# Performance work log

Measured on AMD Instinct MI355X. Metric: run time of the kernel, lower is better.

## Reference

```python
import jax, jax.numpy as jnp
import numpy as np

N_P, N_A, N_T = 20000, 10000, 5000
D_IN, D_OUT = 512, 256
E_P, E_A, E_T = 320000, 160000, 80000


def setup_inputs() -> dict:
    key = jax.random.key(0)
    ks = iter(jax.random.split(key, 64))

    def nrm(shape, scale=1.0):
        return jax.random.normal(next(ks), shape, dtype=jnp.float32) * scale

    def xav(shape):
        # xavier_uniform-like scale (gain 1.414), normal draw is fine for a baseline
        return nrm(shape, 1.414 * (2.0 / (shape[0] + shape[1])) ** 0.5)

    def edges(ne, n_src, n_dst):
        src = jax.random.randint(next(ks), (ne,), 0, n_src, dtype=jnp.int32)
        dst = jax.random.randint(next(ks), (ne,), 0, n_dst, dtype=jnp.int32)
        w = jax.random.uniform(next(ks), (ne,), dtype=jnp.float32) / 16.0  # ~normalized adj values
        return src, dst, w

    d = {}
    d["x_p"] = nrm((N_P, D_IN))
    d["x_a"] = nrm((N_A, D_IN))
    d["x_t"] = nrm((N_T, D_IN))
    d["e_p_a_src"], d["e_p_a_dst"], d["e_p_a_w"] = edges(E_P, N_A, N_P)
    d["e_p_t_src"], d["e_p_t_dst"], d["e_p_t_w"] = edges(E_P, N_T, N_P)
    d["e_a_p_src"], d["e_a_p_dst"], d["e_a_p_w"] = edges(E_A, N_P, N_A)
    d["e_a_t_src"], d["e_a_t_dst"], d["e_a_t_w"] = edges(E_A, N_T, N_A)
    d["e_t_p_src"], d["e_t_p_dst"], d["e_t_p_w"] = edges(E_T, N_P, N_T)
    d["e_t_a_src"], d["e_t_a_dst"], d["e_t_a_w"] = edges(E_T, N_A, N_T)
    # parameters for each target type k: W_proj per neighbor, w_self, w_share, w_att, w_cat, bias
    for k, nbs in (("p", ("a", "t")), ("a", ("p", "t")), ("t", ("p", "a"))):
        for nb in nbs:
            d[f"W_{k}_{nb}"] = xav((D_IN, D_OUT))
        d[f"ws_{k}"] = xav((D_IN, D_OUT))
        d[f"wsh_{k}"] = xav((D_OUT, D_OUT))
        d[f"watt_{k}"] = xav((2 * D_OUT, 1))
        d[f"wcat_{k}"] = xav((2 * D_OUT, D_OUT))
        d[f"b_{k}"] = xav((1, D_OUT))
    return d


def _hete_agg(x_self, w_self, w_share, w_att, w_cat, bias, nb_inputs):
    """nb_inputs: list of (x_nb, W_proj, src, dst, edge_w). Faithful to HeteAggregateLayer."""
    n = x_self.shape[0]
    self_ft = (x_self @ w_self) @ w_share  # [n, d]
    # per-relation: project -> spmm (gather + weighted segment-sum over dst) -> share
    nb_fts = [
        jax.ops.segment_sum((x_nb @ Wp)[src] * ew[:, None], dst, num_segments=n) @ w_share
        for (x_nb, Wp, src, dst, ew) in nb_inputs
    ]
    L = len(nb_fts)
    # e = leaky_relu(cat([cat(nb_ft,0), self_ft.repeat(L,1)],1) @ w_att)  -> [L*n, 1]
    e = jnp.concatenate(
        [jax.nn.leaky_relu(jnp.concatenate([f, self_ft], axis=1) @ w_att) for f in nb_fts],
        axis=0,
    )
    # NOTE: faithful replication of the original `e.view(-1, L)` reshape semantics
    att = jax.nn.softmax(e.reshape(n, L), axis=1)  # [n, L]
    agg = nb_fts[0] * att[:, 0:1]
    for i in range(1, L):
        agg = agg + nb_fts[i] * att[:, i : i + 1]
    return jnp.concatenate([agg, self_ft], axis=1) @ w_cat + bias


def reference(x_p, x_a, x_t,
              e_p_a_src, e_p_a_dst, e_p_a_w, e_p_t_src, e_p_t_dst, e_p_t_w,
              e_a_p_src, e_a_p_dst, e_a_p_w, e_a_t_src, e_a_t_dst, e_a_t_w,
              e_t_p_src, e_t_p_dst, e_t_p_w, e_t_a_src, e_t_a_dst, e_t_a_w,
              W_p_a, W_p_t, ws_p, wsh_p, watt_p, wcat_p, b_p,
              W_a_p, W_a_t, ws_a, wsh_a, watt_a, wcat_a, b_a,
              W_t_p, W_t_a, ws_t, wsh_t, watt_t, wcat_t, b_t):
    out_p = _hete_agg(x_p, ws_p, wsh_p, watt_p, wcat_p, b_p,
                      [(x_a, W_p_a, e_p_a_src, e_p_a_dst, e_p_a_w),
                       (x_t, W_p_t, e_p_t_src, e_p_t_dst, e_p_t_w)])
    out_a = _hete_agg(x_a, ws_a, wsh_a, watt_a, wcat_a, b_a,
                      [(x_p, W_a_p, e_a_p_src, e_a_p_dst, e_a_p_w),
                       (x_t, W_a_t, e_a_t_src, e_a_t_dst, e_a_t_w)])
    out_t = _hete_agg(x_t, ws_t, wsh_t, watt_t, wcat_t, b_t,
                      [(x_p, W_t_p, e_t_p_src, e_t_p_dst, e_t_p_w),
                       (x_a, W_t_a, e_t_a_src, e_t_a_dst, e_t_a_w)])
    return (out_p, out_a, out_t)
```

## Files before the change

### kernel.cpp

```cpp
#include <hip/hip_runtime.h>

namespace {

typedef short s16x8 __attribute__((ext_vector_type(8)));
typedef float f32x4 __attribute__((ext_vector_type(4)));

__device__ __forceinline__ float bf2f(unsigned short u) {
  return __uint_as_float(((unsigned)u) << 16);
}
__device__ __forceinline__ unsigned short f2bf(float f) {
  unsigned u = __float_as_uint(f);
  u += 0x7fffu + ((u >> 16) & 1u);
  return (unsigned short)(u >> 16);
}

struct Tc6 { const float* src[6]; unsigned short* dst[6]; int R[6]; };
__global__ __launch_bounds__(256) void transpose_cvt(Tc6 a) {
  int mat = blockIdx.z;
  int R = a.R[mat];
  int r0 = blockIdx.y * 32, c0 = blockIdx.x * 32;
  if (r0 >= R) return;
  const float* __restrict__ src = a.src[mat];
  unsigned short* __restrict__ dst = a.dst[mat];
  __shared__ float T[32][33];
  int tx = threadIdx.x & 31, ty = threadIdx.x >> 5;
  #pragma unroll
  for (int j = 0; j < 4; ++j) {
    int r = ty + j * 8;
    T[r][tx] = src[(size_t)(r0 + r) * 256 + c0 + tx];
  }
  __syncthreads();
  #pragma unroll
  for (int j = 0; j < 4; ++j) {
    int c = ty + j * 8;
    dst[(size_t)(c0 + c) * R + r0 + tx] = f2bf(T[tx][c]);
  }
}

struct Comb9 { const unsigned short* A[9]; const float* B[9]; unsigned short* C[9]; };
__global__ __launch_bounds__(256) void combine_mfma(Comb9 g) {
  int z = blockIdx.z;
  const unsigned short* __restrict__ A = g.A[z];
  const float* __restrict__ B = g.B[z];
  unsigned short* __restrict__ C = g.C[z];
  int row0 = blockIdx.y * 128;
  int col0 = blockIdx.x * 128;
  __shared__ unsigned short As[128 * 40];
  __shared__ unsigned short Bs[128 * 40];
  int tid = threadIdx.x, lane = tid & 63, w = tid >> 6;
  int quad = lane >> 4, m16 = lane & 15;
  f32x4 acc[2][8];
  #pragma unroll
  for (int r = 0; r < 2; ++r)
    #pragma unroll
    for (int c = 0; c < 8; ++c) acc[r][c] = (f32x4){0.f, 0.f, 0.f, 0.f};
  for (int k0 = 0; k0 < 256; k0 += 32) {
    #pragma unroll
    for (int i = 0; i < 2; ++i) {
      int ch = tid + i * 256;
      int m = ch >> 2, kk = (ch & 3) * 8;
      *(s16x8*)&As[m * 40 + kk] = *(const s16x8*)(A + (size_t)(row0 + m) * 256 + k0 + kk);
      const float4* bp = (const float4*)(B + (size_t)(col0 + m) * 256 + k0 + kk);
      float4 b0 = bp[0], b1 = bp[1];
      s16x8 bv;
      bv[0] = (short)f2bf(b0.x); bv[1] = (short)f2bf(b0.y);
      bv[2] = (short)f2bf(b0.z); bv[3] = (short)f2bf(b0.w);
      bv[4] = (short)f2bf(b1.x); bv[5] = (short)f2bf(b1.y);
      bv[6] = (short)f2bf(b1.z); bv[7] = (short)f2bf(b1.w);
      *(s16x8*)&Bs[m * 40 + kk] = bv;
    }
    __syncthreads();
    s16x8 af[2], bf[8];
    #pragma unroll
    for (int r = 0; r < 2; ++r)
      af[r] = *(const s16x8*)&As[(w * 32 + r * 16 + m16) * 40 + quad * 8];
    #pragma unroll
    for (int c = 0; c < 8; ++c)
      bf[c] = *(const s16x8*)&Bs[(c * 16 + m16) * 40 + quad * 8];
    #pragma unroll
    for (int r = 0; r < 2; ++r)
      #pragma unroll
      for (int c = 0; c < 8; ++c)
        acc[r][c] = __builtin_amdgcn_mfma_f32_16x16x32_bf16(af[r], bf[c], acc[r][c], 0, 0, 0);
    __syncthreads();
  }
  #pragma unroll
  for (int r = 0; r < 2; ++r)
    #pragma unroll
    for (int i = 0; i < 4; ++i) {
      int row = row0 + w * 32 + r * 16 + quad * 4 + i;
      #pragma unroll
      for (int c = 0; c < 8; ++c)
        C[(size_t)row * 512 + col0 + c * 16 + m16] = f2bf(acc[r][c][i]);
    }
}

struct Proj9 { const float* A[9]; const unsigned short* Bt[9]; unsigned short* C[9]; int M[9]; };
__global__ __launch_bounds__(256, 3) void proj_mfma9(Proj9 g) {
  int z = blockIdx.z;
  int M = g.M[z];
  int row0 = blockIdx.y * 64;
  if (row0 >= M) return;
  const float* __restrict__ A = g.A[z];
  const unsigned short* __restrict__ Bt = g.Bt[z];
  unsigned short* __restrict__ C = g.C[z];
  __shared__ unsigned short As[64 * 40];
  __shared__ unsigned short Bs[256 * 40];
  int tid = threadIdx.x, lane = tid & 63, w = tid >> 6;
  int quad = lane >> 4, m16 = lane & 15;
  int am = tid >> 2, akk = (tid & 3) * 8;
  int gr = row0 + am;
  f32x4 acc[4][4];
  #pragma unroll
  for (int r = 0; r < 4; ++r)
    #pragma unroll
    for (int c = 0; c < 4; ++c) acc[r][c] = (f32x4){0.f, 0.f, 0.f, 0.f};

  float4 pa0 = {}, pa1 = {};
  s16x8 pb[4];

  if (gr < M) {
    const float4* ap = (const float4*)(A + (size_t)gr * 512 + akk);
    pa0 = ap[0]; pa1 = ap[1];
  }
  #pragma unroll
  for (int i = 0; i < 4; ++i) {
    int ch = tid + i * 256;
    int m = ch >> 2, kk = (ch & 3) * 8;
    pb[i] = *(const s16x8*)(Bt + (size_t)m * 512 + kk);
  }
  {
    s16x8 v;
    v[0] = (short)f2bf(pa0.x); v[1] = (short)f2bf(pa0.y);
    v[2] = (short)f2bf(pa0.z); v[3] = (short)f2bf(pa0.w);
    v[4] = (short)f2bf(pa1.x); v[5] = (short)f2bf(pa1.y);
    v[6] = (short)f2bf(pa1.z); v[7] = (short)f2bf(pa1.w);
    *(s16x8*)&As[am * 40 + akk] = v;
    #pragma unroll
    for (int i = 0; i < 4; ++i) {
      int ch = tid + i * 256;
      int m = ch >> 2, kk = (ch & 3) * 8;
      *(s16x8*)&Bs[m * 40 + kk] = pb[i];
    }
  }
  __syncthreads();

  for (int k0 = 0; k0 < 512; k0 += 32) {
    int kn = k0 + 32;
    if (kn < 512) {
      if (gr < M) {
        const float4* ap = (const float4*)(A + (size_t)gr * 512 + kn + akk);
        pa0 = ap[0]; pa1 = ap[1];
      }
      #pragma unroll
      for (int i = 0; i < 4; ++i) {
        int ch = tid + i * 256;
        int m = ch >> 2, kk = (ch & 3) * 8;
        pb[i] = *(const s16x8*)(Bt + (size_t)m * 512 + kn + kk);
      }
    }
    s16x8 af[4], bf[4];
    #pragma unroll
    for (int r = 0; r < 4; ++r)
      af[r] = *(const s16x8*)&As[(r * 16 + m16) * 40 + quad * 8];
    #pragma unroll
    for (int c = 0; c < 4; ++c)
      bf[c] = *(const s16x8*)&Bs[(w * 64 + c * 16 + m16) * 40 + quad * 8];
    #pragma unroll
    for (int r = 0; r < 4; ++r)
      #pragma unroll
      for (int c = 0; c < 4; ++c)
        acc[r][c] = __builtin_amdgcn_mfma_f32_16x16x32_bf16(af[r], bf[c], acc[r][c], 0, 0, 0);
    __syncthreads();
    if (kn < 512) {
      s16x8 v;
      v[0] = (short)f2bf(pa0.x); v[1] = (short)f2bf(pa0.y);
      v[2] = (short)f2bf(pa0.z); v[3] = (short)f2bf(pa0.w);
      v[4] = (short)f2bf(pa1.x); v[5] = (short)f2bf(pa1.y);
      v[6] = (short)f2bf(pa1.z); v[7] = (short)f2bf(pa1.w);
      *(s16x8*)&As[am * 40 + akk] = v;
      #pragma unroll
      for (int i = 0; i < 4; ++i) {
        int ch = tid + i * 256;
        int m = ch >> 2, kk = (ch & 3) * 8;
        *(s16x8*)&Bs[m * 40 + kk] = pb[i];
      }
      __syncthreads();
    }
  }
  #pragma unroll
  for (int r = 0; r < 4; ++r)
    #pragma unroll
    for (int i = 0; i < 4; ++i) {
      int row = row0 + r * 16 + quad * 4 + i;
      if (row < M) {
        #pragma unroll
        for (int c = 0; c < 4; ++c)
          C[(size_t)row * 256 + w * 64 + c * 16 + m16] = f2bf(acc[r][c][i]);
      }
    }
}

struct Edges6 { const int* src[6]; const int* dst[6]; const float* w[6]; int nE[6]; int cbase[6]; };

__global__ __launch_bounds__(256) void hist_all(Edges6 ep, int* __restrict__ counts) {
  int rho = blockIdx.y;
  int e = blockIdx.x * 256 + threadIdx.x;
  if (e >= ep.nE[rho]) return;
  atomicAdd(&counts[ep.cbase[rho] + ep.dst[rho][e]], 1);
}

__global__ __launch_bounds__(256) void scan1(const int* __restrict__ cnt, int* __restrict__ out,
                                             int* __restrict__ part, int len) {
  __shared__ int sh[256];
  int base = blockIdx.x * 2048 + threadIdx.x * 8;
  int v[8];
  int s = 0;
  #pragma unroll
  for (int j = 0; j < 8; ++j) {
    int i = base + j;
    int x = (i < len) ? cnt[i] : 0;
    v[j] = s;
    s += x;
  }
  sh[threadIdx.x] = s;
  __syncthreads();
  for (int off = 1; off < 256; off <<= 1) {
    int t = (threadIdx.x >= off) ? sh[threadIdx.x - off] : 0;
    __syncthreads();
    sh[threadIdx.x] += t;
    __syncthreads();
  }
  int texcl = sh[threadIdx.x] - s;
  #pragma unroll
  for (int j = 0; j < 8; ++j) {
    int i = base + j;
    if (i < len) out[i] = texcl + v[j];
  }
  if (threadIdx.x == 255) part[blockIdx.x] = sh[255];
}

__global__ void scan2(int* __restrict__ part, int nb, int* __restrict__ total_out) {
  __shared__ int sh[64];
  int t = threadIdx.x;
  int v = (t < nb) ? part[t] : 0;
  sh[t] = v;
  __syncthreads();
  for (int off = 1; off < 64; off <<= 1) {
    int x = (t >= off) ? sh[t - off] : 0;
    __syncthreads();
    sh[t] += x;
    __syncthreads();
  }
  if (t < nb) part[t] = sh[t] - v;
  if (t == 63) *total_out = sh[63];
}

__global__ __launch_bounds__(256) void scan3(int* __restrict__ offs, int* __restrict__ cursor,
                                             const int* __restrict__ part, int len) {
  int i = blockIdx.x * 256 + threadIdx.x;
  if (i >= len) return;
  int v = offs[i] + part[i >> 11];
  offs[i] = v;
  cursor[i] = v;
}

__global__ __launch_bounds__(256) void fill_all(Edges6 ep, int* __restrict__ cursor,
                                                unsigned int* __restrict__ pay) {
  int rho = blockIdx.y;
  int e = blockIdx.x * 256 + threadIdx.x;
  if (e >= ep.nE[rho]) return;
  int pos = atomicAdd(&cursor[ep.cbase[rho] + ep.dst[rho][e]], 1);
  pay[pos] = (((unsigned)f2bf(ep.w[rho][e])) << 16) | (unsigned)ep.src[rho][e];
}

struct Gather6 { const unsigned short* proj[6]; unsigned short* out[6]; int cb[6]; int n[6]; };
__global__ __launch_bounds__(256) void gather_all(Gather6 g, const int* __restrict__ offs,
                                                  const unsigned int* __restrict__ pay) {
  int rho = blockIdx.y;
  int n = g.n[rho];
  int d = blockIdx.x * 4 + (threadIdx.x >> 6);
  if (d >= n) return;
  int lane = threadIdx.x & 63, half = lane >> 5, l32 = lane & 31;
  const unsigned short* __restrict__ proj = g.proj[rho];
  const int* of = offs + g.cb[rho];
  int s0 = of[d], s1 = of[d + 1];
  float acc[8] = {};
  int e = s0 + half;
  for (; e + 2 < s1; e += 4) {
    unsigned int u0 = pay[e], u1 = pay[e + 2];
    float wt0 = bf2f((unsigned short)(u0 >> 16));
    float wt1 = bf2f((unsigned short)(u1 >> 16));
    s16x8 v0 = *(const s16x8*)(proj + (size_t)(u0 & 0xffffu) * 256 + l32 * 8);
    s16x8 v1 = *(const s16x8*)(proj + (size_t)(u1 & 0xffffu) * 256 + l32 * 8);
    #pragma unroll
    for (int j = 0; j < 8; ++j) {
      acc[j] = fmaf(bf2f((unsigned short)v0[j]), wt0, acc[j]);
      acc[j] = fmaf(bf2f((unsigned short)v1[j]), wt1, acc[j]);
    }
  }
  if (e < s1) {
    unsigned int u = pay[e];
    float wt = bf2f((unsigned short)(u >> 16));
    s16x8 v = *(const s16x8*)(proj + (size_t)(u & 0xffffu) * 256 + l32 * 8);
    #pragma unroll
    for (int j = 0; j < 8; ++j) acc[j] = fmaf(bf2f((unsigned short)v[j]), wt, acc[j]);
  }
  #pragma unroll
  for (int j = 0; j < 8; ++j) acc[j] += __shfl(acc[j], lane ^ 32, 64);
  if (half == 0) {
    s16x8 o;
    #pragma unroll
    for (int j = 0; j < 8; ++j) o[j] = (short)f2bf(acc[j]);
    *(s16x8*)(g.out[rho] + (size_t)d * 256 + l32 * 8) = o;
  }
}

struct Att3 { const unsigned short* nb[3]; const unsigned short* self[3];
              const float* watt[3]; float* att[3]; int n[3]; };
__global__ __launch_bounds__(256) void e_att3(Att3 g) {
  int z = blockIdx.z;
  int n = g.n[z];
  int wv = threadIdx.x >> 6;
  int idx = blockIdx.x * 4 + wv;
  int lane = threadIdx.x & 63;
  __shared__ float ev[4];
  float sum = 0.f;
  if (idx < 2 * n) {
    int i = idx < n ? idx : idx - n;
    ushort4 v  = *(const ushort4*)(g.nb[z] + (size_t)idx * 256 + (lane << 2));
    ushort4 sv = *(const ushort4*)(g.self[z] + (size_t)i * 256 + (lane << 2));
    float4 wa = *(const float4*)(g.watt[z] + (lane << 2));
    float4 wb = *(const float4*)(g.watt[z] + 256 + (lane << 2));
    sum = bf2f(v.x) * wa.x + bf2f(v.y) * wa.y + bf2f(v.z) * wa.z + bf2f(v.w) * wa.w +
          bf2f(sv.x) * wb.x + bf2f(sv.y) * wb.y + bf2f(sv.z) * wb.z + bf2f(sv.w) * wb.w;
    #pragma unroll
    for (int off = 32; off > 0; off >>= 1) sum += __shfl_down(sum, off, 64);
  }
  if (lane == 0) ev[wv] = sum;
  __syncthreads();
  if (threadIdx.x < 2) {
    int base = blockIdx.x * 4 + threadIdx.x * 2;
    if (base < 2 * n) {
      float f0 = ev[threadIdx.x * 2], f1 = ev[threadIdx.x * 2 + 1];
      f0 = f0 > 0.f ? f0 : 0.01f * f0;
      f1 = f1 > 0.f ? f1 : 0.01f * f1;
      float m = fmaxf(f0, f1);
      float a = expf(f0 - m), b = expf(f1 - m);
      float inv = 1.f / (a + b);
      g.att[z][base] = a * inv;
      g.att[z][base + 1] = b * inv;
    }
  }
}

struct Fin3 { const unsigned short* nb[3]; const unsigned short* self[3]; const float* att[3];
              const unsigned short* Wt[3]; const float* bias[3]; float* out[3]; int M[3]; };
__global__ __launch_bounds__(256, 3) void final_mfma3(Fin3 g) {
  int z = blockIdx.z;
  int M = g.M[z];
  int row0 = blockIdx.y * 64;
  if (row0 >= M) return;
  const unsigned short* __restrict__ nbft = g.nb[z];
  const unsigned short* __restrict__ selfb = g.self[z];
  const float* __restrict__ att = g.att[z];
  const unsigned short* __restrict__ Wt = g.Wt[z];
  __shared__ unsigned short As[64 * 40];
  __shared__ unsigned short Bs[256 * 40];
  int tid = threadIdx.x, lane = tid & 63, w = tid >> 6;
  int quad = lane >> 4, m16 = lane & 15;
  int am = tid >> 2, akk = (tid & 3) * 8;
  int gr = row0 + am;
  float a0 = 0.f, a1 = 0.f;
  if (gr < M) { a0 = att[2 * gr]; a1 = att[2 * gr + 1]; }
  f32x4 acc[4][4];
  #pragma unroll
  for (int r = 0; r < 4; ++r)
    #pragma unroll
    for (int c = 0; c < 4; ++c) acc[r][c] = (f32x4){0.f, 0.f, 0.f, 0.f};

  s16x8 pu0 = {}, pu1 = {};
  s16x8 pb[4];

  auto loadA = [&](int k0) {
    int kg = k0 + akk;
    if (gr < M) {
      if (kg < 256) {
        pu0 = *(const s16x8*)(nbft + (size_t)gr * 256 + kg);
        pu1 = *(const s16x8*)(nbft + ((size_t)M + gr) * 256 + kg);
      } else {
        pu0 = *(const s16x8*)(selfb + (size_t)gr * 256 + (kg - 256));
      }
    }
  };
  auto loadB = [&](int k0) {
    #pragma unroll
    for (int i = 0; i < 4; ++i) {
      int ch = tid + i * 256;
      int m = ch >> 2, kk = (ch & 3) * 8;
      pb[i] = *(const s16x8*)(Wt + (size_t)m * 512 + k0 + kk);
    }
  };
  auto storeLDS = [&](int k0) {
    int kg = k0 + akk;
    s16x8 v = {};
    if (gr < M) {
      if (kg < 256) {
        #pragma unroll
        for (int j = 0; j < 8; ++j)
          v[j] = (short)f2bf(fmaf(a0, bf2f((unsigned short)pu0[j]),
                                  a1 * bf2f((unsigned short)pu1[j])));
      } else {
        v = pu0;
      }
    }
    *(s16x8*)&As[am * 40 + akk] = v;
    #pragma unroll
    for (int i = 0; i < 4; ++i) {
      int ch = tid + i * 256;
      int m = ch >> 2, kk = (ch & 3) * 8;
      *(s16x8*)&Bs[m * 40 + kk] = pb[i];
    }
  };

  loadA(0); loadB(0); storeLDS(0);
  __syncthreads();
  for (int k0 = 0; k0 < 512; k0 += 32) {
    int kn = k0 + 32;
    if (kn < 512) { loadA(kn); loadB(kn); }
    s16x8 af[4], bf[4];
    #pragma unroll
    for (int r = 0; r < 4; ++r)
      af[r] = *(const s16x8*)&As[(r * 16 + m16) * 40 + quad * 8];
    #pragma unroll
    for (int c = 0; c < 4; ++c)
      bf[c] = *(const s16x8*)&Bs[(w * 64 + c * 16 + m16) * 40 + quad * 8];
    #pragma unroll
    for (int r = 0; r < 4; ++r)
      #pragma unroll
      for (int c = 0; c < 4; ++c)
        acc[r][c] = __builtin_amdgcn_mfma_f32_16x16x32_bf16(af[r], bf[c], acc[r][c], 0, 0, 0);
    __syncthreads();
    if (kn < 512) {
      storeLDS(kn);
      __syncthreads();
    }
  }
  const float* __restrict__ bias = g.bias[z];
  float* __restrict__ out = g.out[z];
  #pragma unroll
  for (int r = 0; r < 4; ++r)
    #pragma unroll
    for (int i = 0; i < 4; ++i) {
      int row = row0 + r * 16 + quad * 4 + i;
      if (row < M) {
        #pragma unroll
        for (int c = 0; c < 4; ++c) {
          int col = w * 64 + c * 16 + m16;
          out[(size_t)row * 256 + col] = acc[r][c][i] + bias[col];
        }
      }
    }
}

}

extern "C" void kernel_launch(void* const* d_in, const int* in_sizes, int n_in,
                              void* d_out, int out_size, void* d_ws, size_t ws_size,
                              hipStream_t stream) {
  (void)in_sizes; (void)n_in; (void)out_size; (void)ws_size;
  const float* x[3] = {(const float*)d_in[0], (const float*)d_in[1], (const float*)d_in[2]};

  char* p = (char*)d_ws;
  unsigned short* projfull = (unsigned short*)p;  p += (size_t)105000 * 256 * 2;
  unsigned short* nbft = (unsigned short*)p;      p += (size_t)70000 * 256 * 2;
  unsigned short* wcatbt = (unsigned short*)p;    p += (size_t)3 * 256 * 512 * 2;
  int* offs = (int*)p;                            p += (size_t)70004 * 4;
  int* counts = (int*)p;                          p += (size_t)70000 * 4;
  int* part = (int*)p;                            p += 256;
  float* att_buf = (float*)p;                     p += (size_t)70000 * 4;
  unsigned int* csr_pay = (unsigned int*)p;       p += (size_t)1120000 * 4;
  unsigned short* wshT = nbft;
  unsigned short* Wcbt = (unsigned short*)((char*)nbft + 393216);

  const int n_of[3] = {20000, 10000, 5000};
  const int nbt[3][2] = {{1, 2}, {0, 2}, {0, 1}};
  const int ebase[3][2] = {{3, 6}, {9, 12}, {15, 18}};
  const int nE3[3] = {320000, 160000, 80000};
  const size_t out_off[3] = {0, (size_t)20000 * 256, (size_t)30000 * 256};
  const int tstart[3] = {0, 15000, 40000};
  const int selfoff[3] = {70000, 90000, 100000};
  const int nboff[3] = {0, 40000, 60000};

  Tc6 tc;
  for (int t = 0; t < 3; ++t) {
    tc.src[t] = (const float*)d_in[21 + t * 7 + 3];
    tc.dst[t] = wshT + (size_t)t * 256 * 256;
    tc.R[t] = 256;
    tc.src[3 + t] = (const float*)d_in[21 + t * 7 + 5];
    tc.dst[3 + t] = wcatbt + (size_t)t * 256 * 512;
    tc.R[3 + t] = 512;
  }
  transpose_cvt<<<dim3(8, 16, 6), 256, 0, stream>>>(tc);

  Comb9 c9;
  for (int t = 0; t < 3; ++t) {
    int wb = 21 + t * 7;
    for (int j = 0; j < 3; ++j) {
      int combo = t * 3 + j;
      c9.A[combo] = wshT + (size_t)t * 256 * 256;
      c9.B[combo] = (const float*)d_in[wb + j];
      c9.C[combo] = Wcbt + (size_t)combo * 256 * 512;
    }
  }
  combine_mfma<<<dim3(4, 2, 9), 256, 0, stream>>>(c9);

  Edges6 ep;
  const int cbase[6] = {0, 20000, 40000, 50000, 60000, 65000};
  for (int t = 0; t < 3; ++t)
    for (int r = 0; r < 2; ++r) {
      int rho = t * 2 + r, eb = ebase[t][r];
      ep.src[rho] = (const int*)d_in[eb];
      ep.dst[rho] = (const int*)d_in[eb + 1];
      ep.w[rho] = (const float*)d_in[eb + 2];
      ep.nE[rho] = nE3[t];
      ep.cbase[rho] = cbase[rho];
    }
  hipMemsetAsync(counts, 0, (size_t)70000 * 4, stream);
  hist_all<<<dim3(1250, 6), 256, 0, stream>>>(ep, counts);
  scan1<<<35, 256, 0, stream>>>(counts, offs, part, 70000);
  scan2<<<1, 64, 0, stream>>>(part, 35, offs + 70000);
  scan3<<<274, 256, 0, stream>>>(offs, counts, part, 70000);
  fill_all<<<dim3(1250, 6), 256, 0, stream>>>(ep, counts, csr_pay);

  Proj9 pj;
  for (int t = 0; t < 3; ++t) {
    int nb0 = nbt[t][0], nb1 = nbt[t][1];
    int m0 = n_of[nb0];
    pj.A[t * 3 + 0] = x[nb0];
    pj.C[t * 3 + 0] = projfull + (size_t)tstart[t] * 256;
    pj.M[t * 3 + 0] = m0;
    pj.A[t * 3 + 1] = x[nb1];
    pj.C[t * 3 + 1] = projfull + (size_t)(tstart[t] + m0) * 256;
    pj.M[t * 3 + 1] = n_of[nb1];
    pj.A[t * 3 + 2] = x[t];
    pj.C[t * 3 + 2] = projfull + (size_t)selfoff[t] * 256;
    pj.M[t * 3 + 2] = n_of[t];
    for (int j = 0; j < 3; ++j)
      pj.Bt[t * 3 + j] = Wcbt + (size_t)(t * 3 + j) * 256 * 512;
  }
  proj_mfma9<<<dim3(1, 313, 9), 256, 0, stream>>>(pj);

  Gather6 gt;
  for (int t = 0; t < 3; ++t) {
    int m0 = n_of[nbt[t][0]];
    for (int r = 0; r < 2; ++r) {
      int rho = t * 2 + r;
      gt.proj[rho] = projfull + (size_t)(tstart[t] + (r ? m0 : 0)) * 256;
      gt.out[rho] = nbft + (size_t)(nboff[t] + r * n_of[t]) * 256;
      gt.cb[rho] = cbase[rho];
      gt.n[rho] = n_of[t];
    }
  }
  gather_all<<<dim3(5000, 6), 256, 0, stream>>>(gt, offs, csr_pay);

  Att3 at;
  for (int t = 0; t < 3; ++t) {
    at.nb[t] = nbft + (size_t)nboff[t] * 256;
    at.self[t] = projfull + (size_t)selfoff[t] * 256;
    at.watt[t] = (const float*)d_in[21 + t * 7 + 4];
    at.att[t] = att_buf + nboff[t];
    at.n[t] = n_of[t];
  }
  e_att3<<<dim3(10000, 1, 3), 256, 0, stream>>>(at);

  Fin3 fn;
  for (int t = 0; t < 3; ++t) {
    fn.nb[t] = nbft + (size_t)nboff[t] * 256;
    fn.self[t] = projfull + (size_t)selfoff[t] * 256;
    fn.att[t] = att_buf + nboff[t];
    fn.Wt[t] = wcatbt + (size_t)t * 256 * 512;
    fn.bias[t] = (const float*)d_in[21 + t * 7 + 6];
    fn.out[t] = (float*)d_out + out_off[t];
    fn.M[t] = n_of[t];
  }
  final_mfma3<<<dim3(1, 313, 3), 256, 0, stream>>>(fn);
}
```

Before: 475.2 us.

## Pre-convert inputs to bf16 and restructure projection GEMM with direct LDS loads

Adds a kernel that converts all three node feature matrices to bf16 once, staging them in the output buffer as scratch, instead of converting fp32 to bf16 inside every projection tile. The projection GEMM moves from 64x256 tiles to 128x128 tiles over a 2D grid and loads A and B tiles straight into LDS with global_load_lds. The register-prefetch double buffering and padded LDS rows are removed. Each x is now read once at fp32 and several times at half width, at the cost of an extra launch, an unpipelined load-then-compute loop, and possible LDS bank conflicts from the unpadded layout.

```diff
diff --git a/kernel.cpp b/kernel.cpp
--- a/kernel.cpp
+++ b/kernel.cpp
@@ -12,6 +12,32 @@
   unsigned u = __float_as_uint(f);
   u += 0x7fffu + ((u >> 16) & 1u);
   return (unsigned short)(u >> 16);
+}
+
+typedef __attribute__((address_space(3))) unsigned int lds_u32;
+typedef __attribute__((address_space(1))) const unsigned int glob_u32;
+__device__ __forceinline__ void gl16(const void* g, void* l) {
+  __builtin_amdgcn_global_load_lds((glob_u32*)g, (lds_u32*)l, 16, 0, 0);
+}
+
+__global__ __launch_bounds__(256) void cvt_x3(const float* __restrict__ x0,
+                                              const float* __restrict__ x1,
+                                              const float* __restrict__ x2,
+                                              unsigned short* __restrict__ out) {
+  size_t i = ((size_t)blockIdx.x * 256 + threadIdx.x) * 8;
+  const float* src;
+  size_t off;
+  if (i < (size_t)20000 * 512) { src = x0; off = i; }
+  else if (i < (size_t)30000 * 512) { src = x1; off = i - (size_t)20000 * 512; }
+  else { src = x2; off = i - (size_t)30000 * 512; }
+  float4 a = *(const float4*)(src + off);
+  float4 b = *(const float4*)(src + off + 4);
+  s16x8 v;
+  v[0] = (short)f2bf(a.x); v[1] = (short)f2bf(a.y);
+  v[2] = (short)f2bf(a.z); v[3] = (short)f2bf(a.w);
+  v[4] = (short)f2bf(b.x); v[5] = (short)f2bf(b.y);
+  v[6] = (short)f2bf(b.z); v[7] = (short)f2bf(b.w);
+  *(s16x8*)(out + i) = v;
 }
 
 struct Tc6 { const float* src[6]; unsigned short* dst[6]; int R[6]; };
@@ -95,108 +121,66 @@
     }
 }
 
-struct Proj9 { const float* A[9]; const unsigned short* Bt[9]; unsigned short* C[9]; int M[9]; };
-__global__ __launch_bounds__(256, 3) void proj_mfma9(Proj9 g) {
+struct Proj9 { const unsigned short* A[9]; const unsigned short* Bt[9]; unsigned short* C[9]; int M[9]; };
+__global__ __launch_bounds__(256) void proj_mfma9(Proj9 g) {
   int z = blockIdx.z;
   int M = g.M[z];
-  int row0 = blockIdx.y * 64;
+  int row0 = blockIdx.y * 128;
   if (row0 >= M) return;
-  const float* __restrict__ A = g.A[z];
+  int col0 = blockIdx.x * 128;
+  const unsigned short* __restrict__ A = g.A[z];
   const unsigned short* __restrict__ Bt = g.Bt[z];
   unsigned short* __restrict__ C = g.C[z];
-  __shared__ unsigned short As[64 * 40];
-  __shared__ unsigned short Bs[256 * 40];
+  __shared__ unsigned short As[128 * 32];
+  __shared__ unsigned short Bs[128 * 32];
   int tid = threadIdx.x, lane = tid & 63, w = tid >> 6;
   int quad = lane >> 4, m16 = lane & 15;
-  int am = tid >> 2, akk = (tid & 3) * 8;
-  int gr = row0 + am;
+  int lr = lane >> 2, lk = (lane & 3) * 8;
+  int r0g = row0 + w * 32 + lr;
+  int r1g = r0g + 16;
+  const unsigned short* a0p = A + (size_t)(r0g < M ? r0g : M - 1) * 512 + lk;
+  const unsigned short* a1p = A + (size_t)(r1g < M ? r1g : M - 1) * 512 + lk;
+  const unsigned short* b0p = Bt + (size_t)(col0 + w * 32 + lr) * 512 + lk;
+  const unsigned short* b1p = b0p + (size_t)16 * 512;
+  unsigned short* as0 = &As[w * 1024];
+  unsigned short* as1 = &As[w * 1024 + 512];
+  unsigned short* bs0 = &Bs[w * 1024];
+  unsigned short* bs1 = &Bs[w * 1024 + 512];
+  int wr = (w & 1) * 64, wc = (w >> 1) * 64;
   f32x4 acc[4][4];
   #pragma unroll
   for (int r = 0; r < 4; ++r)
     #pragma unroll
     for (int c = 0; c < 4; ++c) acc[r][c] = (f32x4){0.f, 0.f, 0.f, 0.f};
-
-  float4 pa0 = {}, pa1 = {};
-  s16x8 pb[4];
-
-  if (gr < M) {
-    const float4* ap = (const float4*)(A + (size_t)gr * 512 + akk);
-    pa0 = ap[0]; pa1 = ap[1];
-  }
-  #pragma unroll
-  for (int i = 0; i < 4; ++i) {
-    int ch = tid + i * 256;
-    int m = ch >> 2, kk = (ch & 3) * 8;
-    pb[i] = *(const s16x8*)(Bt + (size_t)m * 512 + kk);
-  }
-  {
-    s16x8 v;
-    v[0] = (short)f2bf(pa0.x); v[1] = (short)f2bf(pa0.y);
-    v[2] = (short)f2bf(pa0.z); v[3] = (short)f2bf(pa0.w);
-    v[4] = (short)f2bf(pa1.x); v[5] = (short)f2bf(pa1.y);
-    v[6] = (short)f2bf(pa1.z); v[7] = (short)f2bf(pa1.w);
-    *(s16x8*)&As[am * 40 + akk] = v;
-    #pragma unroll
-    for (int i = 0; i < 4; ++i) {
-      int ch = tid + i * 256;
-      int m = ch >> 2, kk = (ch & 3) * 8;
-      *(s16x8*)&Bs[m * 40 + kk] = pb[i];
-    }
-  }
-  __syncthreads();
-
   for (int k0 = 0; k0 < 512; k0 += 32) {
-    int kn = k0 + 32;
-    if (kn < 512) {
-      if (gr < M) {
-        const float4* ap = (const float4*)(A + (size_t)gr * 512 + kn + akk);
-        pa0 = ap[0]; pa1 = ap[1];
-      }
-      #pragma unroll
-      for (int i = 0; i < 4; ++i) {
-        int ch = tid + i * 256;
-        int m = ch >> 2, kk = (ch & 3) * 8;
-        pb[i] = *(const s16x8*)(Bt + (size_t)m * 512 + kn + kk);
-      }
-    }
+    gl16(a0p + k0, as0);
+    gl16(a1p + k0, as1);
+    gl16(b0p + k0, bs0);
+    gl16(b1p + k0, bs1);
+    __syncthreads();
     s16x8 af[4], bf[4];
     #pragma unroll
     for (int r = 0; r < 4; ++r)
-      af[r] = *(const s16x8*)&As[(r * 16 + m16) * 40 + quad * 8];
+      af[r] = *(const s16x8*)&As[(wr + r * 16 + m16) * 32 + quad * 8];
     #pragma unroll
     for (int c = 0; c < 4; ++c)
-      bf[c] = *(const s16x8*)&Bs[(w * 64 + c * 16 + m16) * 40 + quad * 8];
+      bf[c] = *(const s16x8*)&Bs[(wc + c * 16 + m16) * 32 + quad * 8];
     #pragma unroll
     for (int r = 0; r < 4; ++r)
       #pragma unroll
       for (int c = 0; c < 4; ++c)
         acc[r][c] = __builtin_amdgcn_mfma_f32_16x16x32_bf16(af[r], bf[c], acc[r][c], 0, 0, 0);
     __syncthreads();
-    if (kn < 512) {
-      s16x8 v;
-      v[0] = (short)f2bf(pa0.x); v[1] = (short)f2bf(pa0.y);
-      v[2] = (short)f2bf(pa0.z); v[3] = (short)f2bf(pa0.w);
-      v[4] = (short)f2bf(pa1.x); v[5] = (short)f2bf(pa1.y);
-      v[6] = (short)f2bf(pa1.z); v[7] = (short)f2bf(pa1.w);
-      *(s16x8*)&As[am * 40 + akk] = v;
-      #pragma unroll
-      for (int i = 0; i < 4; ++i) {
-        int ch = tid + i * 256;
-        int m = ch >> 2, kk = (ch & 3) * 8;
-        *(s16x8*)&Bs[m * 40 + kk] = pb[i];
-      }
-      __syncthreads();
-    }
   }
   #pragma unroll
   for (int r = 0; r < 4; ++r)
     #pragma unroll
     for (int i = 0; i < 4; ++i) {
-      int row = row0 + r * 16 + quad * 4 + i;
+      int row = row0 + wr + r * 16 + quad * 4 + i;
       if (row < M) {
         #pragma unroll
         for (int c = 0; c < 4; ++c)
-          C[(size_t)row * 256 + w * 64 + c * 16 + m16] = f2bf(acc[r][c][i]);
+          C[(size_t)row * 256 + col0 + wc + c * 16 + m16] = f2bf(acc[r][c][i]);
       }
     }
 }
@@ -482,6 +466,7 @@
   unsigned int* csr_pay = (unsigned int*)p;       p += (size_t)1120000 * 4;
   unsigned short* wshT = nbft;
   unsigned short* Wcbt = (unsigned short*)((char*)nbft + 393216);
+  unsigned short* xb = (unsigned short*)d_out;
 
   const int n_of[3] = {20000, 10000, 5000};
   const int nbt[3][2] = {{1, 2}, {0, 2}, {0, 1}};
@@ -491,6 +476,9 @@
   const int tstart[3] = {0, 15000, 40000};
   const int selfoff[3] = {70000, 90000, 100000};
   const int nboff[3] = {0, 40000, 60000};
+  const int xboff[3] = {0, 20000, 30000};
+
+  cvt_x3<<<dim3(8750), 256, 0, stream>>>(x[0], x[1], x[2], xb);
 
   Tc6 tc;
   for (int t = 0; t < 3; ++t) {
@@ -537,19 +525,19 @@
   for (int t = 0; t < 3; ++t) {
     int nb0 = nbt[t][0], nb1 = nbt[t][1];
     int m0 = n_of[nb0];
-    pj.A[t * 3 + 0] = x[nb0];
+    pj.A[t * 3 + 0] = xb + (size_t)xboff[nb0] * 512;
     pj.C[t * 3 + 0] = projfull + (size_t)tstart[t] * 256;
     pj.M[t * 3 + 0] = m0;
-    pj.A[t * 3 + 1] = x[nb1];
+    pj.A[t * 3 + 1] = xb + (size_t)xboff[nb1] * 512;
     pj.C[t * 3 + 1] = projfull + (size_t)(tstart[t] + m0) * 256;
     pj.M[t * 3 + 1] = n_of[nb1];
-    pj.A[t * 3 + 2] = x[t];
+    pj.A[t * 3 + 2] = xb + (size_t)xboff[t] * 512;
     pj.C[t * 3 + 2] = projfull + (size_t)selfoff[t] * 256;
     pj.M[t * 3 + 2] = n_of[t];
     for (int j = 0; j < 3; ++j)
       pj.Bt[t * 3 + j] = Wcbt + (size_t)(t * 3 + j) * 256 * 512;
   }
-  proj_mfma9<<<dim3(1, 313, 9), 256, 0, stream>>>(pj);
+  proj_mfma9<<<dim3(2, 157, 9), 256, 0, stream>>>(pj);
 
   Gather6 gt;
   for (int t = 0; t < 3; ++t) {
```

Result: slower. 485.5 us (+2.2%).
